# Optimization experiments

Measured on AMD Instinct MI355X. Metric: run time of the kernel, lower is better.

Reference implementation:

```python
import jax, jax.numpy as jnp
import numpy as np

BETA = 0.25
N_E = 4096
E_DIM = 64
B, T = 16, 1024


def setup_inputs() -> dict:
    key = jax.random.key(0)
    k1, k2 = jax.random.split(key)
    z = jax.random.normal(k1, (B, T, E_DIM), dtype=jnp.float32)
    # embedding.weight.data.uniform_(-1/n_e, 1/n_e)
    codebook = jax.random.uniform(k2, (N_E, E_DIM), dtype=jnp.float32,
                                  minval=-1.0 / N_E, maxval=1.0 / N_E)
    return {"z": z, "codebook": codebook}


def reference(z, codebook):
    # z: (B, T, e_dim), codebook: (n_e, e_dim)
    n_e, e_dim = codebook.shape
    zf = z.reshape(-1, e_dim)  # (N, e_dim)

    # d[n, k] = ||z_n||^2 + ||e_k||^2 - 2 z_n . e_k   -> (N, n_e)
    d = (jnp.sum(zf * zf, axis=1, keepdims=True)
         + jnp.sum(codebook * codebook, axis=1)
         - 2.0 * jnp.matmul(zf, codebook.T))

    idx = jnp.argmin(d, axis=1)                  # (N,) int
    z_q = codebook[idx].reshape(z.shape)         # (B, T, e_dim)

    sg = jax.lax.stop_gradient
    loss = jnp.mean((z_q - sg(z)) ** 2) + BETA * jnp.mean((sg(z_q) - z) ** 2)

    # straight-through estimator
    z_q_st = z + sg(z_q - z)

    # e_mean = mean over tokens of one-hot encodings == normalized code counts
    n_tokens = idx.shape[0]
    counts = jnp.zeros((n_e,), dtype=z.dtype).at[idx].add(1.0)
    e_mean = counts / n_tokens
    perplexity = jnp.exp(-jnp.sum(e_mean * jnp.log(e_mean + 1e-10)))

    return (loss, z_q_st, idx, perplexity)
```

## Files before the change

### kernel.cpp

```cpp
#include <hip/hip_runtime.h>
#include <math.h>

#define N_TOK   16384
#define EDIM    64
#define NE      4096
#define CHUNK   128
#define TPB     256
#define TOKPT   2
#define ZQ_OFF  1
#define IDX_OFF (1 + N_TOK * EDIM)
#define PERP_OFF (IDX_OFF + N_TOK)

typedef unsigned long long u64;
typedef float v2f __attribute__((ext_vector_type(2)));
typedef float v4f __attribute__((ext_vector_type(4)));

__global__ __launch_bounds__(256, 2) void dist_argmin_kernel(
    const float* __restrict__ z, const float* __restrict__ cb,
    u64* __restrict__ part, int* __restrict__ hist,
    float* __restrict__ lossAcc, int csl) {
    __shared__ float se[CHUNK * EDIM];
    __shared__ float sne[CHUNK];
    const int tid    = threadIdx.x;
    const int token0 = blockIdx.x * (TPB * TOKPT) + tid;
    const int token1 = token0 + TPB;
    const int slice  = blockIdx.y;

    if (slice == 0) {
        int gid = blockIdx.x * TPB + tid;
        if (gid < NE) hist[gid] = 0;
        if (gid == NE) lossAcc[0] = 0.0f;
    }

    v2f zp[EDIM];
    {
        const v4f* zp0 = (const v4f*)(z + (size_t)token0 * EDIM);
        const v4f* zp1 = (const v4f*)(z + (size_t)token1 * EDIM);
#pragma unroll
        for (int q = 0; q < 16; ++q) {
            v4f a = zp0[q], b = zp1[q];
            zp[4 * q + 0].x = a.x; zp[4 * q + 0].y = b.x;
            zp[4 * q + 1].x = a.y; zp[4 * q + 1].y = b.y;
            zp[4 * q + 2].x = a.z; zp[4 * q + 2].y = b.z;
            zp[4 * q + 3].x = a.w; zp[4 * q + 3].y = b.w;
        }
    }
    float tnz0, tnz1;
    {
#pragma clang fp contract(off)
        float r0[8], r1[8];
#pragma unroll
        for (int j = 0; j < 8; ++j) {
            float v0 = zp[j].x, v1 = zp[j].y;
            r0[j] = v0 * v0; r1[j] = v1 * v1;
        }
#pragma unroll
        for (int b = 8; b < 64; b += 8) {
#pragma unroll
            for (int j = 0; j < 8; ++j) {
                float v0 = zp[b + j].x, v1 = zp[b + j].y;
                r0[j] = r0[j] + v0 * v0; r1[j] = r1[j] + v1 * v1;
            }
        }
        tnz0 = ((r0[0] + r0[1]) + (r0[2] + r0[3])) + ((r0[4] + r0[5]) + (r0[6] + r0[7]));
        tnz1 = ((r1[0] + r1[1]) + (r1[2] + r1[3])) + ((r1[4] + r1[5]) + (r1[6] + r1[7]));
    }

    u64 best0 = ~0ull, best1 = ~0ull;
    const int kend = slice * csl + csl;
#pragma unroll 1
    for (int kbase = slice * csl; kbase < kend; kbase += CHUNK) {
        {
            const v4f* src = (const v4f*)(cb + (size_t)kbase * EDIM);
            v4f* dst = (v4f*)se;
#pragma unroll
            for (int r = 0; r < (CHUNK * EDIM / 4) / TPB; ++r)
                dst[r * TPB + tid] = src[r * TPB + tid];
        }
        if (tid < CHUNK) {
#pragma clang fp contract(off)
            const v4f* cr = (const v4f*)(cb + (size_t)(kbase + tid) * EDIM);
            float r[8];
            {
                v4f c0 = cr[0], c1 = cr[1];
                r[0] = c0.x * c0.x; r[1] = c0.y * c0.y;
                r[2] = c0.z * c0.z; r[3] = c0.w * c0.w;
                r[4] = c1.x * c1.x; r[5] = c1.y * c1.y;
                r[6] = c1.z * c1.z; r[7] = c1.w * c1.w;
            }
#pragma unroll
            for (int b = 1; b < 8; ++b) {
                v4f a = cr[2 * b], d = cr[2 * b + 1];
                r[0] = r[0] + a.x * a.x; r[1] = r[1] + a.y * a.y;
                r[2] = r[2] + a.z * a.z; r[3] = r[3] + a.w * a.w;
                r[4] = r[4] + d.x * d.x; r[5] = r[5] + d.y * d.y;
                r[6] = r[6] + d.z * d.z; r[7] = r[7] + d.w * d.w;
            }
            sne[tid] = ((r[0] + r[1]) + (r[2] + r[3])) + ((r[4] + r[5]) + (r[6] + r[7]));
        }
        __syncthreads();

#pragma unroll 1
        for (int k = 0; k < CHUNK; k += 2) {
            const v4f* e0 = (const v4f*)(se + (size_t)(k + 0) * EDIM);
            const v4f* e1 = (const v4f*)(se + (size_t)(k + 1) * EDIM);
            v2f a0 = {0.f, 0.f}, a1 = {0.f, 0.f};
#pragma unroll
            for (int q = 0; q < 16; ++q) {
                v4f A = e0[q], B = e1[q];
                v2f Alo = __builtin_shufflevector(A, A, 0, 1);
                v2f Ahi = __builtin_shufflevector(A, A, 2, 3);
                v2f Blo = __builtin_shufflevector(B, B, 0, 1);
                v2f Bhi = __builtin_shufflevector(B, B, 2, 3);
                asm("v_pk_fma_f32 %0, %1, %2, %0 op_sel:[0,0,0] op_sel_hi:[1,0,1]"
                    : "+v"(a0) : "v"(zp[4 * q + 0]), "v"(Alo));
                asm("v_pk_fma_f32 %0, %1, %2, %0 op_sel:[0,1,0] op_sel_hi:[1,1,1]"
                    : "+v"(a0) : "v"(zp[4 * q + 1]), "v"(Alo));
                asm("v_pk_fma_f32 %0, %1, %2, %0 op_sel:[0,0,0] op_sel_hi:[1,0,1]"
                    : "+v"(a0) : "v"(zp[4 * q + 2]), "v"(Ahi));
                asm("v_pk_fma_f32 %0, %1, %2, %0 op_sel:[0,1,0] op_sel_hi:[1,1,1]"
                    : "+v"(a0) : "v"(zp[4 * q + 3]), "v"(Ahi));
                asm("v_pk_fma_f32 %0, %1, %2, %0 op_sel:[0,0,0] op_sel_hi:[1,0,1]"
                    : "+v"(a1) : "v"(zp[4 * q + 0]), "v"(Blo));
                asm("v_pk_fma_f32 %0, %1, %2, %0 op_sel:[0,1,0] op_sel_hi:[1,1,1]"
                    : "+v"(a1) : "v"(zp[4 * q + 1]), "v"(Blo));
                asm("v_pk_fma_f32 %0, %1, %2, %0 op_sel:[0,0,0] op_sel_hi:[1,0,1]"
                    : "+v"(a1) : "v"(zp[4 * q + 2]), "v"(Bhi));
                asm("v_pk_fma_f32 %0, %1, %2, %0 op_sel:[0,1,0] op_sel_hi:[1,1,1]"
                    : "+v"(a1) : "v"(zp[4 * q + 3]), "v"(Bhi));
            }
            const float s0 = sne[k + 0], s1 = sne[k + 1];
            float t00 = __builtin_fmaf(-2.0f, a0.x, tnz0 + s0);
            float t01 = __builtin_fmaf(-2.0f, a1.x, tnz0 + s1);
            float t10 = __builtin_fmaf(-2.0f, a0.y, tnz1 + s0);
            float t11 = __builtin_fmaf(-2.0f, a1.y, tnz1 + s1);
            u64 p;
            p = ((u64)__float_as_uint(t00) << 32) | (u64)(kbase + k + 0); if (p < best0) best0 = p;
            p = ((u64)__float_as_uint(t01) << 32) | (u64)(kbase + k + 1); if (p < best0) best0 = p;
            p = ((u64)__float_as_uint(t10) << 32) | (u64)(kbase + k + 0); if (p < best1) best1 = p;
            p = ((u64)__float_as_uint(t11) << 32) | (u64)(kbase + k + 1); if (p < best1) best1 = p;
        }
        __syncthreads();
    }
    part[(size_t)slice * N_TOK + token0] = best0;
    part[(size_t)slice * N_TOK + token1] = best1;
}

__global__ __launch_bounds__(256) void reduce_gather_kernel(
    const float* __restrict__ z, const float* __restrict__ cb,
    const u64* __restrict__ part, int* __restrict__ hist,
    float* __restrict__ lossAcc, float* __restrict__ out, int nslice) {
    const int t = blockIdx.x * 256 + threadIdx.x;
    u64 best = part[t];
    for (int s = 1; s < nslice; ++s) {
        u64 p = part[(size_t)s * N_TOK + t];
        if (p < best) best = p;
    }
    const int idx = (int)(best & 0xFFFFFFFFull);
    out[IDX_OFF + t] = (float)idx;
    atomicAdd(&hist[idx], 1);

    const float4* ev = (const float4*)(cb + (size_t)idx * EDIM);
    const float4* zv = (const float4*)(z + (size_t)t * EDIM);
    float* o = out + ZQ_OFF + (size_t)t * EDIM;
    float acc = 0.0f;
#pragma unroll
    for (int j = 0; j < 16; ++j) {
        float4 e = ev[j], zz = zv[j];
        float d;
        d = e.x - zz.x; o[4 * j + 0] = zz.x + d; acc = __builtin_fmaf(d, d, acc);
        d = e.y - zz.y; o[4 * j + 1] = zz.y + d; acc = __builtin_fmaf(d, d, acc);
        d = e.z - zz.z; o[4 * j + 2] = zz.z + d; acc = __builtin_fmaf(d, d, acc);
        d = e.w - zz.w; o[4 * j + 3] = zz.w + d; acc = __builtin_fmaf(d, d, acc);
    }
    __shared__ float red[256];
    red[threadIdx.x] = acc;
    __syncthreads();
    for (int s = 128; s > 0; s >>= 1) {
        if (threadIdx.x < s) red[threadIdx.x] += red[threadIdx.x + s];
        __syncthreads();
    }
    if (threadIdx.x == 0) atomicAdd(lossAcc, red[0]);
}

__global__ __launch_bounds__(256) void finalize_kernel(
    const int* __restrict__ hist, const float* __restrict__ lossAcc,
    float* __restrict__ out) {
    __shared__ float red[256];
    float acc = 0.0f;
    for (int i = threadIdx.x; i < NE; i += 256) {
        float e = (float)hist[i] * (1.0f / 16384.0f);
        acc += e * logf(e + 1e-10f);
    }
    red[threadIdx.x] = acc;
    __syncthreads();
    for (int s = 128; s > 0; s >>= 1) {
        if (threadIdx.x < s) red[threadIdx.x] += red[threadIdx.x + s];
        __syncthreads();
    }
    if (threadIdx.x == 0) {
        out[PERP_OFF] = expf(-red[0]);
        float m = lossAcc[0] * (1.0f / 1048576.0f);
        out[0] = m + 0.25f * m;
    }
}

extern "C" void kernel_launch(void* const* d_in, const int* in_sizes, int n_in,
                              void* d_out, int out_size, void* d_ws, size_t ws_size,
                              hipStream_t stream) {
    const float* z  = (const float*)d_in[0];
    const float* cb = (const float*)d_in[1];
    float* out = (float*)d_out;

    const size_t need32 = (size_t)32 * N_TOK * 8 + (size_t)(NE + 1) * 4;
    const int nslice = (ws_size >= need32) ? 32 : 16;
    const int csl = NE / nslice;

    char* ws = (char*)d_ws;
    u64*   part    = (u64*)ws;
    int*   hist    = (int*)(ws + (size_t)nslice * N_TOK * 8);
    float* lossAcc = (float*)(hist + NE);

    hipLaunchKernelGGL(dist_argmin_kernel,
                       dim3(N_TOK / (TPB * TOKPT), nslice), dim3(TPB), 0, stream,
                       z, cb, part, hist, lossAcc, csl);
    hipLaunchKernelGGL(reduce_gather_kernel, dim3(64), dim3(256), 0, stream,
                       z, cb, part, hist, lossAcc, out, nslice);
    hipLaunchKernelGGL(finalize_kernel, dim3(1), dim3(256), 0, stream,
                       hist, lossAcc, out);
}
```

Before: 225.2 us.

## Register-block four tokens per thread and parallelize gather across quarter-rows

The distance kernel now holds four tokens per thread in registers instead of two. Each shared-memory codebook load therefore feeds twice as many packed FMAs. The chunk loop is dropped on the assumption that each slice covers exactly one CHUNK of codes. The reduce/gather kernel splits each token across four threads, each handling 16 elements, which gives more blocks and better-coalesced work. Risks: holding 256 z values per thread may exceed the VGPR budget under launch_bounds(256,2) and spill. The distance grid is halved, and the 16-slice fallback would skip half of each slice's codes.

```diff
diff --git a/kernel.cpp b/kernel.cpp
--- a/kernel.cpp
+++ b/kernel.cpp
@@ -6,7 +6,7 @@
 #define NE      4096
 #define CHUNK   128
 #define TPB     256
-#define TOKPT   2
+#define TOKPT   4
 #define ZQ_OFF  1
 #define IDX_OFF (1 + N_TOK * EDIM)
 #define PERP_OFF (IDX_OFF + N_TOK)
@@ -18,160 +18,190 @@
 __global__ __launch_bounds__(256, 2) void dist_argmin_kernel(
     const float* __restrict__ z, const float* __restrict__ cb,
     u64* __restrict__ part, int* __restrict__ hist,
-    float* __restrict__ lossAcc, int csl) {
+    float* __restrict__ lossAcc, int nslice) {
     __shared__ float se[CHUNK * EDIM];
     __shared__ float sne[CHUNK];
     const int tid    = threadIdx.x;
     const int token0 = blockIdx.x * (TPB * TOKPT) + tid;
-    const int token1 = token0 + TPB;
     const int slice  = blockIdx.y;
+    const int kb     = slice * (NE / nslice);
 
     if (slice == 0) {
         int gid = blockIdx.x * TPB + tid;
         if (gid < NE) hist[gid] = 0;
-        if (gid == NE) lossAcc[0] = 0.0f;
-    }
-
-    v2f zp[EDIM];
+        if (gid == 0) lossAcc[0] = 0.0f;
+    }
+
+    v2f zpA[EDIM], zpB[EDIM];
     {
-        const v4f* zp0 = (const v4f*)(z + (size_t)token0 * EDIM);
-        const v4f* zp1 = (const v4f*)(z + (size_t)token1 * EDIM);
+        const v4f* p0 = (const v4f*)(z + (size_t)(token0 + 0 * TPB) * EDIM);
+        const v4f* p1 = (const v4f*)(z + (size_t)(token0 + 1 * TPB) * EDIM);
+        const v4f* p2 = (const v4f*)(z + (size_t)(token0 + 2 * TPB) * EDIM);
+        const v4f* p3 = (const v4f*)(z + (size_t)(token0 + 3 * TPB) * EDIM);
 #pragma unroll
         for (int q = 0; q < 16; ++q) {
-            v4f a = zp0[q], b = zp1[q];
-            zp[4 * q + 0].x = a.x; zp[4 * q + 0].y = b.x;
-            zp[4 * q + 1].x = a.y; zp[4 * q + 1].y = b.y;
-            zp[4 * q + 2].x = a.z; zp[4 * q + 2].y = b.z;
-            zp[4 * q + 3].x = a.w; zp[4 * q + 3].y = b.w;
-        }
-    }
-    float tnz0, tnz1;
+            v4f a = p0[q], b = p1[q], c = p2[q], d = p3[q];
+            zpA[4 * q + 0].x = a.x; zpA[4 * q + 0].y = b.x;
+            zpA[4 * q + 1].x = a.y; zpA[4 * q + 1].y = b.y;
+            zpA[4 * q + 2].x = a.z; zpA[4 * q + 2].y = b.z;
+            zpA[4 * q + 3].x = a.w; zpA[4 * q + 3].y = b.w;
+            zpB[4 * q + 0].x = c.x; zpB[4 * q + 0].y = d.x;
+            zpB[4 * q + 1].x = c.y; zpB[4 * q + 1].y = d.y;
+            zpB[4 * q + 2].x = c.z; zpB[4 * q + 2].y = d.z;
+            zpB[4 * q + 3].x = c.w; zpB[4 * q + 3].y = d.w;
+        }
+    }
+    float tnz0, tnz1, tnz2, tnz3;
     {
 #pragma clang fp contract(off)
-        float r0[8], r1[8];
+        float r0[8], r1[8], r2[8], r3[8];
 #pragma unroll
         for (int j = 0; j < 8; ++j) {
-            float v0 = zp[j].x, v1 = zp[j].y;
-            r0[j] = v0 * v0; r1[j] = v1 * v1;
-        }
-#pragma unroll
-        for (int b = 8; b < 64; b += 8) {
+            float a = zpA[j].x, b = zpA[j].y, c = zpB[j].x, d = zpB[j].y;
+            r0[j] = a * a; r1[j] = b * b; r2[j] = c * c; r3[j] = d * d;
+        }
+#pragma unroll
+        for (int bb = 8; bb < 64; bb += 8) {
 #pragma unroll
             for (int j = 0; j < 8; ++j) {
-                float v0 = zp[b + j].x, v1 = zp[b + j].y;
-                r0[j] = r0[j] + v0 * v0; r1[j] = r1[j] + v1 * v1;
+                float a = zpA[bb + j].x, b = zpA[bb + j].y;
+                float c = zpB[bb + j].x, d = zpB[bb + j].y;
+                r0[j] = r0[j] + a * a; r1[j] = r1[j] + b * b;
+                r2[j] = r2[j] + c * c; r3[j] = r3[j] + d * d;
             }
         }
         tnz0 = ((r0[0] + r0[1]) + (r0[2] + r0[3])) + ((r0[4] + r0[5]) + (r0[6] + r0[7]));
         tnz1 = ((r1[0] + r1[1]) + (r1[2] + r1[3])) + ((r1[4] + r1[5]) + (r1[6] + r1[7]));
-    }
-
-    u64 best0 = ~0ull, best1 = ~0ull;
-    const int kend = slice * csl + csl;
+        tnz2 = ((r2[0] + r2[1]) + (r2[2] + r2[3])) + ((r2[4] + r2[5]) + (r2[6] + r2[7]));
+        tnz3 = ((r3[0] + r3[1]) + (r3[2] + r3[3])) + ((r3[4] + r3[5]) + (r3[6] + r3[7]));
+    }
+
+    {
+        const v4f* src = (const v4f*)(cb + (size_t)kb * EDIM);
+        v4f* dst = (v4f*)se;
+#pragma unroll
+        for (int r = 0; r < (CHUNK * EDIM / 4) / TPB; ++r)
+            dst[r * TPB + tid] = src[r * TPB + tid];
+    }
+    if (tid < CHUNK) {
+#pragma clang fp contract(off)
+        const v4f* cr = (const v4f*)(cb + (size_t)(kb + tid) * EDIM);
+        float r[8];
+        {
+            v4f c0 = cr[0], c1 = cr[1];
+            r[0] = c0.x * c0.x; r[1] = c0.y * c0.y;
+            r[2] = c0.z * c0.z; r[3] = c0.w * c0.w;
+            r[4] = c1.x * c1.x; r[5] = c1.y * c1.y;
+            r[6] = c1.z * c1.z; r[7] = c1.w * c1.w;
+        }
+#pragma unroll
+        for (int b = 1; b < 8; ++b) {
+            v4f a = cr[2 * b], d = cr[2 * b + 1];
+            r[0] = r[0] + a.x * a.x; r[1] = r[1] + a.y * a.y;
+            r[2] = r[2] + a.z * a.z; r[3] = r[3] + a.w * a.w;
+            r[4] = r[4] + d.x * d.x; r[5] = r[5] + d.y * d.y;
+            r[6] = r[6] + d.z * d.z; r[7] = r[7] + d.w * d.w;
+        }
+        sne[tid] = ((r[0] + r[1]) + (r[2] + r[3])) + ((r[4] + r[5]) + (r[6] + r[7]));
+    }
+    __syncthreads();
+
+    u64 best0 = ~0ull, best1 = ~0ull, best2 = ~0ull, best3 = ~0ull;
 #pragma unroll 1
-    for (int kbase = slice * csl; kbase < kend; kbase += CHUNK) {
-        {
-            const v4f* src = (const v4f*)(cb + (size_t)kbase * EDIM);
-            v4f* dst = (v4f*)se;
-#pragma unroll
-            for (int r = 0; r < (CHUNK * EDIM / 4) / TPB; ++r)
-                dst[r * TPB + tid] = src[r * TPB + tid];
-        }
-        if (tid < CHUNK) {
-#pragma clang fp contract(off)
-            const v4f* cr = (const v4f*)(cb + (size_t)(kbase + tid) * EDIM);
-            float r[8];
-            {
-                v4f c0 = cr[0], c1 = cr[1];
-                r[0] = c0.x * c0.x; r[1] = c0.y * c0.y;
-                r[2] = c0.z * c0.z; r[3] = c0.w * c0.w;
-                r[4] = c1.x * c1.x; r[5] = c1.y * c1.y;
-                r[6] = c1.z * c1.z; r[7] = c1.w * c1.w;
-            }
-#pragma unroll
-            for (int b = 1; b < 8; ++b) {
-                v4f a = cr[2 * b], d = cr[2 * b + 1];
-                r[0] = r[0] + a.x * a.x; r[1] = r[1] + a.y * a.y;
-                r[2] = r[2] + a.z * a.z; r[3] = r[3] + a.w * a.w;
-                r[4] = r[4] + d.x * d.x; r[5] = r[5] + d.y * d.y;
-                r[6] = r[6] + d.z * d.z; r[7] = r[7] + d.w * d.w;
-            }
-            sne[tid] = ((r[0] + r[1]) + (r[2] + r[3])) + ((r[4] + r[5]) + (r[6] + r[7]));
-        }
-        __syncthreads();
-
-#pragma unroll 1
-        for (int k = 0; k < CHUNK; k += 2) {
-            const v4f* e0 = (const v4f*)(se + (size_t)(k + 0) * EDIM);
-            const v4f* e1 = (const v4f*)(se + (size_t)(k + 1) * EDIM);
-            v2f a0 = {0.f, 0.f}, a1 = {0.f, 0.f};
-#pragma unroll
-            for (int q = 0; q < 16; ++q) {
-                v4f A = e0[q], B = e1[q];
-                v2f Alo = __builtin_shufflevector(A, A, 0, 1);
-                v2f Ahi = __builtin_shufflevector(A, A, 2, 3);
-                v2f Blo = __builtin_shufflevector(B, B, 0, 1);
-                v2f Bhi = __builtin_shufflevector(B, B, 2, 3);
-                asm("v_pk_fma_f32 %0, %1, %2, %0 op_sel:[0,0,0] op_sel_hi:[1,0,1]"
-                    : "+v"(a0) : "v"(zp[4 * q + 0]), "v"(Alo));
-                asm("v_pk_fma_f32 %0, %1, %2, %0 op_sel:[0,1,0] op_sel_hi:[1,1,1]"
-                    : "+v"(a0) : "v"(zp[4 * q + 1]), "v"(Alo));
-                asm("v_pk_fma_f32 %0, %1, %2, %0 op_sel:[0,0,0] op_sel_hi:[1,0,1]"
-                    : "+v"(a0) : "v"(zp[4 * q + 2]), "v"(Ahi));
-                asm("v_pk_fma_f32 %0, %1, %2, %0 op_sel:[0,1,0] op_sel_hi:[1,1,1]"
-                    : "+v"(a0) : "v"(zp[4 * q + 3]), "v"(Ahi));
-                asm("v_pk_fma_f32 %0, %1, %2, %0 op_sel:[0,0,0] op_sel_hi:[1,0,1]"
-                    : "+v"(a1) : "v"(zp[4 * q + 0]), "v"(Blo));
-                asm("v_pk_fma_f32 %0, %1, %2, %0 op_sel:[0,1,0] op_sel_hi:[1,1,1]"
-                    : "+v"(a1) : "v"(zp[4 * q + 1]), "v"(Blo));
-                asm("v_pk_fma_f32 %0, %1, %2, %0 op_sel:[0,0,0] op_sel_hi:[1,0,1]"
-                    : "+v"(a1) : "v"(zp[4 * q + 2]), "v"(Bhi));
-                asm("v_pk_fma_f32 %0, %1, %2, %0 op_sel:[0,1,0] op_sel_hi:[1,1,1]"
-                    : "+v"(a1) : "v"(zp[4 * q + 3]), "v"(Bhi));
-            }
-            const float s0 = sne[k + 0], s1 = sne[k + 1];
-            float t00 = __builtin_fmaf(-2.0f, a0.x, tnz0 + s0);
-            float t01 = __builtin_fmaf(-2.0f, a1.x, tnz0 + s1);
-            float t10 = __builtin_fmaf(-2.0f, a0.y, tnz1 + s0);
-            float t11 = __builtin_fmaf(-2.0f, a1.y, tnz1 + s1);
-            u64 p;
-            p = ((u64)__float_as_uint(t00) << 32) | (u64)(kbase + k + 0); if (p < best0) best0 = p;
-            p = ((u64)__float_as_uint(t01) << 32) | (u64)(kbase + k + 1); if (p < best0) best0 = p;
-            p = ((u64)__float_as_uint(t10) << 32) | (u64)(kbase + k + 0); if (p < best1) best1 = p;
-            p = ((u64)__float_as_uint(t11) << 32) | (u64)(kbase + k + 1); if (p < best1) best1 = p;
-        }
-        __syncthreads();
-    }
-    part[(size_t)slice * N_TOK + token0] = best0;
-    part[(size_t)slice * N_TOK + token1] = best1;
+    for (int k = 0; k < CHUNK; k += 2) {
+        const v4f* e0 = (const v4f*)(se + (size_t)(k + 0) * EDIM);
+        const v4f* e1 = (const v4f*)(se + (size_t)(k + 1) * EDIM);
+        v2f aA0 = {0.f, 0.f}, aA1 = {0.f, 0.f};
+        v2f aB0 = {0.f, 0.f}, aB1 = {0.f, 0.f};
+#pragma unroll
+        for (int q = 0; q < 16; ++q) {
+            v4f A = e0[q], B = e1[q];
+            v2f Alo = __builtin_shufflevector(A, A, 0, 1);
+            v2f Ahi = __builtin_shufflevector(A, A, 2, 3);
+            v2f Blo = __builtin_shufflevector(B, B, 0, 1);
+            v2f Bhi = __builtin_shufflevector(B, B, 2, 3);
+            asm("v_pk_fma_f32 %0, %1, %2, %0 op_sel:[0,0,0] op_sel_hi:[1,0,1]"
+                : "+v"(aA0) : "v"(zpA[4 * q + 0]), "v"(Alo));
+            asm("v_pk_fma_f32 %0, %1, %2, %0 op_sel:[0,1,0] op_sel_hi:[1,1,1]"
+                : "+v"(aA0) : "v"(zpA[4 * q + 1]), "v"(Alo));
+            asm("v_pk_fma_f32 %0, %1, %2, %0 op_sel:[0,0,0] op_sel_hi:[1,0,1]"
+                : "+v"(aA0) : "v"(zpA[4 * q + 2]), "v"(Ahi));
+            asm("v_pk_fma_f32 %0, %1, %2, %0 op_sel:[0,1,0] op_sel_hi:[1,1,1]"
+                : "+v"(aA0) : "v"(zpA[4 * q + 3]), "v"(Ahi));
+            asm("v_pk_fma_f32 %0, %1, %2, %0 op_sel:[0,0,0] op_sel_hi:[1,0,1]"
+                : "+v"(aA1) : "v"(zpA[4 * q + 0]), "v"(Blo));
+            asm("v_pk_fma_f32 %0, %1, %2, %0 op_sel:[0,1,0] op_sel_hi:[1,1,1]"
+                : "+v"(aA1) : "v"(zpA[4 * q + 1]), "v"(Blo));
+            asm("v_pk_fma_f32 %0, %1, %2, %0 op_sel:[0,0,0] op_sel_hi:[1,0,1]"
+                : "+v"(aA1) : "v"(zpA[4 * q + 2]), "v"(Bhi));
+            asm("v_pk_fma_f32 %0, %1, %2, %0 op_sel:[0,1,0] op_sel_hi:[1,1,1]"
+                : "+v"(aA1) : "v"(zpA[4 * q + 3]), "v"(Bhi));
+            asm("v_pk_fma_f32 %0, %1, %2, %0 op_sel:[0,0,0] op_sel_hi:[1,0,1]"
+                : "+v"(aB0) : "v"(zpB[4 * q + 0]), "v"(Alo));
+            asm("v_pk_fma_f32 %0, %1, %2, %0 op_sel:[0,1,0] op_sel_hi:[1,1,1]"
+                : "+v"(aB0) : "v"(zpB[4 * q + 1]), "v"(Alo));
+            asm("v_pk_fma_f32 %0, %1, %2, %0 op_sel:[0,0,0] op_sel_hi:[1,0,1]"
+                : "+v"(aB0) : "v"(zpB[4 * q + 2]), "v"(Ahi));
+            asm("v_pk_fma_f32 %0, %1, %2, %0 op_sel:[0,1,0] op_sel_hi:[1,1,1]"
+                : "+v"(aB0) : "v"(zpB[4 * q + 3]), "v"(Ahi));
+            asm("v_pk_fma_f32 %0, %1, %2, %0 op_sel:[0,0,0] op_sel_hi:[1,0,1]"
+                : "+v"(aB1) : "v"(zpB[4 * q + 0]), "v"(Blo));
+            asm("v_pk_fma_f32 %0, %1, %2, %0 op_sel:[0,1,0] op_sel_hi:[1,1,1]"
+                : "+v"(aB1) : "v"(zpB[4 * q + 1]), "v"(Blo));
+            asm("v_pk_fma_f32 %0, %1, %2, %0 op_sel:[0,0,0] op_sel_hi:[1,0,1]"
+                : "+v"(aB1) : "v"(zpB[4 * q + 2]), "v"(Bhi));
+            asm("v_pk_fma_f32 %0, %1, %2, %0 op_sel:[0,1,0] op_sel_hi:[1,1,1]"
+                : "+v"(aB1) : "v"(zpB[4 * q + 3]), "v"(Bhi));
+        }
+        const float s0 = sne[k + 0], s1 = sne[k + 1];
+        float t00 = __builtin_fmaf(-2.f, aA0.x, tnz0 + s0);
+        float t10 = __builtin_fmaf(-2.f, aA0.y, tnz1 + s0);
+        float t20 = __builtin_fmaf(-2.f, aB0.x, tnz2 + s0);
+        float t30 = __builtin_fmaf(-2.f, aB0.y, tnz3 + s0);
+        float t01 = __builtin_fmaf(-2.f, aA1.x, tnz0 + s1);
+        float t11 = __builtin_fmaf(-2.f, aA1.y, tnz1 + s1);
+        float t21 = __builtin_fmaf(-2.f, aB1.x, tnz2 + s1);
+        float t31 = __builtin_fmaf(-2.f, aB1.y, tnz3 + s1);
+        u64 p;
+        p = ((u64)__float_as_uint(t00) << 32) | (u64)(kb + k + 0); if (p < best0) best0 = p;
+        p = ((u64)__float_as_uint(t01) << 32) | (u64)(kb + k + 1); if (p < best0) best0 = p;
+        p = ((u64)__float_as_uint(t10) << 32) | (u64)(kb + k + 0); if (p < best1) best1 = p;
+        p = ((u64)__float_as_uint(t11) << 32) | (u64)(kb + k + 1); if (p < best1) best1 = p;
+        p = ((u64)__float_as_uint(t20) << 32) | (u64)(kb + k + 0); if (p < best2) best2 = p;
+        p = ((u64)__float_as_uint(t21) << 32) | (u64)(kb + k + 1); if (p < best2) best2 = p;
+        p = ((u64)__float_as_uint(t30) << 32) | (u64)(kb + k + 0); if (p < best3) best3 = p;
+        p = ((u64)__float_as_uint(t31) << 32) | (u64)(kb + k + 1); if (p < best3) best3 = p;
+    }
+    part[(size_t)slice * N_TOK + token0 + 0 * TPB] = best0;
+    part[(size_t)slice * N_TOK + token0 + 1 * TPB] = best1;
+    part[(size_t)slice * N_TOK + token0 + 2 * TPB] = best2;
+    part[(size_t)slice * N_TOK + token0 + 3 * TPB] = best3;
 }
 
 __global__ __launch_bounds__(256) void reduce_gather_kernel(
     const float* __restrict__ z, const float* __restrict__ cb,
     const u64* __restrict__ part, int* __restrict__ hist,
     float* __restrict__ lossAcc, float* __restrict__ out, int nslice) {
-    const int t = blockIdx.x * 256 + threadIdx.x;
-    u64 best = part[t];
+    const int id = blockIdx.x * 256 + threadIdx.x;
+    const int tok = id >> 2, q = id & 3;
+    u64 best = part[tok];
     for (int s = 1; s < nslice; ++s) {
-        u64 p = part[(size_t)s * N_TOK + t];
+        u64 p = part[(size_t)s * N_TOK + tok];
         if (p < best) best = p;
     }
     const int idx = (int)(best & 0xFFFFFFFFull);
-    out[IDX_OFF + t] = (float)idx;
-    atomicAdd(&hist[idx], 1);
-
-    const float4* ev = (const float4*)(cb + (size_t)idx * EDIM);
-    const float4* zv = (const float4*)(z + (size_t)t * EDIM);
-    float* o = out + ZQ_OFF + (size_t)t * EDIM;
-    float acc = 0.0f;
-#pragma unroll
-    for (int j = 0; j < 16; ++j) {
-        float4 e = ev[j], zz = zv[j];
-        float d;
-        d = e.x - zz.x; o[4 * j + 0] = zz.x + d; acc = __builtin_fmaf(d, d, acc);
-        d = e.y - zz.y; o[4 * j + 1] = zz.y + d; acc = __builtin_fmaf(d, d, acc);
-        d = e.z - zz.z; o[4 * j + 2] = zz.z + d; acc = __builtin_fmaf(d, d, acc);
-        d = e.w - zz.w; o[4 * j + 3] = zz.w + d; acc = __builtin_fmaf(d, d, acc);
+    if (q == 0) { out[IDX_OFF + tok] = (float)idx; atomicAdd(&hist[idx], 1); }
+
+    const float* ev = cb + (size_t)idx * EDIM + 16 * q;
+    const float* zv = z + (size_t)tok * EDIM + 16 * q;
+    float* o = out + ZQ_OFF + (size_t)tok * EDIM + 16 * q;
+    float acc = 0.f;
+#pragma unroll
+    for (int i = 0; i < 16; ++i) {
+        float e = ev[i], zz = zv[i];
+        float d = e - zz;
+        o[i] = zz + d;
+        acc = __builtin_fmaf(d, d, acc);
     }
     __shared__ float red[256];
     red[threadIdx.x] = acc;
@@ -214,7 +244,6 @@
 
     const size_t need32 = (size_t)32 * N_TOK * 8 + (size_t)(NE + 1) * 4;
     const int nslice = (ws_size >= need32) ? 32 : 16;
-    const int csl = NE / nslice;
 
     char* ws = (char*)d_ws;
     u64*   part    = (u64*)ws;
@@ -223,8 +252,8 @@
 
     hipLaunchKernelGGL(dist_argmin_kernel,
                        dim3(N_TOK / (TPB * TOKPT), nslice), dim3(TPB), 0, stream,
-                       z, cb, part, hist, lossAcc, csl);
-    hipLaunchKernelGGL(reduce_gather_kernel, dim3(64), dim3(256), 0, stream,
+                       z, cb, part, hist, lossAcc, nslice);
+    hipLaunchKernelGGL(reduce_gather_kernel, dim3(256), dim3(256), 0, stream,
                        z, cb, part, hist, lossAcc, out, nslice);
     hipLaunchKernelGGL(finalize_kernel, dim3(1), dim3(256), 0, stream,
                        hist, lossAcc, out);
```

New measurement: 359.4 us. 59.5% more time.

## Read codebook via scalar loads, precompute code norms, widen gather parallelism

Applied to the files above, without the earlier changes.

The distance kernel no longer stages codebook chunks in LDS behind barriers. Codebook rows are block-uniform, so it reads them through scalar (SGPR) loads that feed packed FMAs directly. Code norms are now computed once by a new prep kernel, which also zeroes the histogram and loss accumulator. The slice count drops from 32 to 16, and the gather kernel uses four threads per token for more parallelism. This removes LDS traffic and synchronisation, but the hot loop now depends on scalar-cache latency, and there are fewer blocks plus one extra launch.

```diff
diff --git a/kernel.cpp b/kernel.cpp
--- a/kernel.cpp
+++ b/kernel.cpp
@@ -4,7 +4,6 @@
 #define N_TOK   16384
 #define EDIM    64
 #define NE      4096
-#define CHUNK   128
 #define TPB     256
 #define TOKPT   2
 #define ZQ_OFF  1
@@ -15,30 +14,40 @@
 typedef float v2f __attribute__((ext_vector_type(2)));
 typedef float v4f __attribute__((ext_vector_type(4)));
 
+__global__ __launch_bounds__(256) void prep_kernel(
+    const float* __restrict__ cb, float* __restrict__ ne,
+    int* __restrict__ hist, float* __restrict__ lossAcc) {
+#pragma clang fp contract(off)
+    const int i = blockIdx.x * 256 + threadIdx.x;
+    hist[i] = 0;
+    if (i == 0) lossAcc[0] = 0.0f;
+    const float* row = cb + (size_t)i * EDIM;
+    float r[8];
+#pragma unroll
+    for (int j = 0; j < 8; ++j) { float v = row[j]; r[j] = v * v; }
+#pragma unroll
+    for (int b = 8; b < 64; b += 8) {
+#pragma unroll
+        for (int j = 0; j < 8; ++j) { float v = row[b + j]; r[j] = r[j] + v * v; }
+    }
+    ne[i] = ((r[0] + r[1]) + (r[2] + r[3])) + ((r[4] + r[5]) + (r[6] + r[7]));
+}
+
 __global__ __launch_bounds__(256, 2) void dist_argmin_kernel(
     const float* __restrict__ z, const float* __restrict__ cb,
-    u64* __restrict__ part, int* __restrict__ hist,
-    float* __restrict__ lossAcc, int csl) {
-    __shared__ float se[CHUNK * EDIM];
-    __shared__ float sne[CHUNK];
+    const float* __restrict__ ne, u64* __restrict__ part, int csl) {
     const int tid    = threadIdx.x;
     const int token0 = blockIdx.x * (TPB * TOKPT) + tid;
     const int token1 = token0 + TPB;
-    const int slice  = blockIdx.y;
-
-    if (slice == 0) {
-        int gid = blockIdx.x * TPB + tid;
-        if (gid < NE) hist[gid] = 0;
-        if (gid == NE) lossAcc[0] = 0.0f;
-    }
+    const int kb     = __builtin_amdgcn_readfirstlane(blockIdx.y * csl);
 
     v2f zp[EDIM];
     {
-        const v4f* zp0 = (const v4f*)(z + (size_t)token0 * EDIM);
-        const v4f* zp1 = (const v4f*)(z + (size_t)token1 * EDIM);
+        const v4f* p0 = (const v4f*)(z + (size_t)token0 * EDIM);
+        const v4f* p1 = (const v4f*)(z + (size_t)token1 * EDIM);
 #pragma unroll
         for (int q = 0; q < 16; ++q) {
-            v4f a = zp0[q], b = zp1[q];
+            v4f a = p0[q], b = p1[q];
             zp[4 * q + 0].x = a.x; zp[4 * q + 0].y = b.x;
             zp[4 * q + 1].x = a.y; zp[4 * q + 1].y = b.y;
             zp[4 * q + 2].x = a.z; zp[4 * q + 2].y = b.z;
@@ -51,15 +60,15 @@
         float r0[8], r1[8];
 #pragma unroll
         for (int j = 0; j < 8; ++j) {
-            float v0 = zp[j].x, v1 = zp[j].y;
-            r0[j] = v0 * v0; r1[j] = v1 * v1;
+            float a = zp[j].x, b = zp[j].y;
+            r0[j] = a * a; r1[j] = b * b;
         }
 #pragma unroll
-        for (int b = 8; b < 64; b += 8) {
+        for (int bb = 8; bb < 64; bb += 8) {
 #pragma unroll
             for (int j = 0; j < 8; ++j) {
-                float v0 = zp[b + j].x, v1 = zp[b + j].y;
-                r0[j] = r0[j] + v0 * v0; r1[j] = r1[j] + v1 * v1;
+                float a = zp[bb + j].x, b = zp[bb + j].y;
+                r0[j] = r0[j] + a * a; r1[j] = r1[j] + b * b;
             }
         }
         tnz0 = ((r0[0] + r0[1]) + (r0[2] + r0[3])) + ((r0[4] + r0[5]) + (r0[6] + r0[7]));
@@ -67,111 +76,64 @@
     }
 
     u64 best0 = ~0ull, best1 = ~0ull;
-    const int kend = slice * csl + csl;
 #pragma unroll 1
-    for (int kbase = slice * csl; kbase < kend; kbase += CHUNK) {
-        {
-            const v4f* src = (const v4f*)(cb + (size_t)kbase * EDIM);
-            v4f* dst = (v4f*)se;
+    for (int kk = 0; kk < csl; kk += 2) {
+        const int k = kb + kk;
+        const u64* e0 = (const u64*)(cb + (size_t)(k + 0) * EDIM);
+        const u64* e1 = (const u64*)(cb + (size_t)(k + 1) * EDIM);
+        v2f a0 = {0.f, 0.f}, a1 = {0.f, 0.f};
 #pragma unroll
-            for (int r = 0; r < (CHUNK * EDIM / 4) / TPB; ++r)
-                dst[r * TPB + tid] = src[r * TPB + tid];
+        for (int jp = 0; jp < 32; ++jp) {
+            u64 w0 = e0[jp];
+            u64 w1 = e1[jp];
+            asm("v_pk_fma_f32 %0, %1, %2, %0 op_sel:[0,0,0] op_sel_hi:[1,0,1]"
+                : "+v"(a0) : "v"(zp[2 * jp + 0]), "s"(w0));
+            asm("v_pk_fma_f32 %0, %1, %2, %0 op_sel:[0,1,0] op_sel_hi:[1,1,1]"
+                : "+v"(a0) : "v"(zp[2 * jp + 1]), "s"(w0));
+            asm("v_pk_fma_f32 %0, %1, %2, %0 op_sel:[0,0,0] op_sel_hi:[1,0,1]"
+                : "+v"(a1) : "v"(zp[2 * jp + 0]), "s"(w1));
+            asm("v_pk_fma_f32 %0, %1, %2, %0 op_sel:[0,1,0] op_sel_hi:[1,1,1]"
+                : "+v"(a1) : "v"(zp[2 * jp + 1]), "s"(w1));
         }
-        if (tid < CHUNK) {
-#pragma clang fp contract(off)
-            const v4f* cr = (const v4f*)(cb + (size_t)(kbase + tid) * EDIM);
-            float r[8];
-            {
-                v4f c0 = cr[0], c1 = cr[1];
-                r[0] = c0.x * c0.x; r[1] = c0.y * c0.y;
-                r[2] = c0.z * c0.z; r[3] = c0.w * c0.w;
-                r[4] = c1.x * c1.x; r[5] = c1.y * c1.y;
-                r[6] = c1.z * c1.z; r[7] = c1.w * c1.w;
-            }
-#pragma unroll
-            for (int b = 1; b < 8; ++b) {
-                v4f a = cr[2 * b], d = cr[2 * b + 1];
-                r[0] = r[0] + a.x * a.x; r[1] = r[1] + a.y * a.y;
-                r[2] = r[2] + a.z * a.z; r[3] = r[3] + a.w * a.w;
-                r[4] = r[4] + d.x * d.x; r[5] = r[5] + d.y * d.y;
-                r[6] = r[6] + d.z * d.z; r[7] = r[7] + d.w * d.w;
-            }
-            sne[tid] = ((r[0] + r[1]) + (r[2] + r[3])) + ((r[4] + r[5]) + (r[6] + r[7]));
-        }
-        __syncthreads();
-
-#pragma unroll 1
-        for (int k = 0; k < CHUNK; k += 2) {
-            const v4f* e0 = (const v4f*)(se + (size_t)(k + 0) * EDIM);
-            const v4f* e1 = (const v4f*)(se + (size_t)(k + 1) * EDIM);
-            v2f a0 = {0.f, 0.f}, a1 = {0.f, 0.f};
-#pragma unroll
-            for (int q = 0; q < 16; ++q) {
-                v4f A = e0[q], B = e1[q];
-                v2f Alo = __builtin_shufflevector(A, A, 0, 1);
-                v2f Ahi = __builtin_shufflevector(A, A, 2, 3);
-                v2f Blo = __builtin_shufflevector(B, B, 0, 1);
-                v2f Bhi = __builtin_shufflevector(B, B, 2, 3);
-                asm("v_pk_fma_f32 %0, %1, %2, %0 op_sel:[0,0,0] op_sel_hi:[1,0,1]"
-                    : "+v"(a0) : "v"(zp[4 * q + 0]), "v"(Alo));
-                asm("v_pk_fma_f32 %0, %1, %2, %0 op_sel:[0,1,0] op_sel_hi:[1,1,1]"
-                    : "+v"(a0) : "v"(zp[4 * q + 1]), "v"(Alo));
-                asm("v_pk_fma_f32 %0, %1, %2, %0 op_sel:[0,0,0] op_sel_hi:[1,0,1]"
-                    : "+v"(a0) : "v"(zp[4 * q + 2]), "v"(Ahi));
-                asm("v_pk_fma_f32 %0, %1, %2, %0 op_sel:[0,1,0] op_sel_hi:[1,1,1]"
-                    : "+v"(a0) : "v"(zp[4 * q + 3]), "v"(Ahi));
-                asm("v_pk_fma_f32 %0, %1, %2, %0 op_sel:[0,0,0] op_sel_hi:[1,0,1]"
-                    : "+v"(a1) : "v"(zp[4 * q + 0]), "v"(Blo));
-                asm("v_pk_fma_f32 %0, %1, %2, %0 op_sel:[0,1,0] op_sel_hi:[1,1,1]"
-                    : "+v"(a1) : "v"(zp[4 * q + 1]), "v"(Blo));
-                asm("v_pk_fma_f32 %0, %1, %2, %0 op_sel:[0,0,0] op_sel_hi:[1,0,1]"
-                    : "+v"(a1) : "v"(zp[4 * q + 2]), "v"(Bhi));
-                asm("v_pk_fma_f32 %0, %1, %2, %0 op_sel:[0,1,0] op_sel_hi:[1,1,1]"
-                    : "+v"(a1) : "v"(zp[4 * q + 3]), "v"(Bhi));
-            }
-            const float s0 = sne[k + 0], s1 = sne[k + 1];
-            float t00 = __builtin_fmaf(-2.0f, a0.x, tnz0 + s0);
-            float t01 = __builtin_fmaf(-2.0f, a1.x, tnz0 + s1);
-            float t10 = __builtin_fmaf(-2.0f, a0.y, tnz1 + s0);
-            float t11 = __builtin_fmaf(-2.0f, a1.y, tnz1 + s1);
-            u64 p;
-            p = ((u64)__float_as_uint(t00) << 32) | (u64)(kbase + k + 0); if (p < best0) best0 = p;
-            p = ((u64)__float_as_uint(t01) << 32) | (u64)(kbase + k + 1); if (p < best0) best0 = p;
-            p = ((u64)__float_as_uint(t10) << 32) | (u64)(kbase + k + 0); if (p < best1) best1 = p;
-            p = ((u64)__float_as_uint(t11) << 32) | (u64)(kbase + k + 1); if (p < best1) best1 = p;
-        }
-        __syncthreads();
+        const float s0 = ne[k], s1 = ne[k + 1];
+        float t00 = __builtin_fmaf(-2.f, a0.x, tnz0 + s0);
+        float t10 = __builtin_fmaf(-2.f, a0.y, tnz1 + s0);
+        float t01 = __builtin_fmaf(-2.f, a1.x, tnz0 + s1);
+        float t11 = __builtin_fmaf(-2.f, a1.y, tnz1 + s1);
+        u64 p;
+        p = ((u64)__float_as_uint(t00) << 32) | (u64)(k + 0); if (p < best0) best0 = p;
+        p = ((u64)__float_as_uint(t01) << 32) | (u64)(k + 1); if (p < best0) best0 = p;
+        p = ((u64)__float_as_uint(t10) << 32) | (u64)(k + 0); if (p < best1) best1 = p;
+        p = ((u64)__float_as_uint(t11) << 32) | (u64)(k + 1); if (p < best1) best1 = p;
     }
-    part[(size_t)slice * N_TOK + token0] = best0;
-    part[(size_t)slice * N_TOK + token1] = best1;
+    part[(size_t)blockIdx.y * N_TOK + token0] = best0;
+    part[(size_t)blockIdx.y * N_TOK + token1] = best1;
 }
 
 __global__ __launch_bounds__(256) void reduce_gather_kernel(
     const float* __restrict__ z, const float* __restrict__ cb,
     const u64* __restrict__ part, int* __restrict__ hist,
     float* __restrict__ lossAcc, float* __restrict__ out, int nslice) {
-    const int t = blockIdx.x * 256 + threadIdx.x;
-    u64 best = part[t];
+    const int id = blockIdx.x * 256 + threadIdx.x;
+    const int tok = id >> 2, q = id & 3;
+    u64 best = part[tok];
     for (int s = 1; s < nslice; ++s) {
-        u64 p = part[(size_t)s * N_TOK + t];
+        u64 p = part[(size_t)s * N_TOK + tok];
         if (p < best) best = p;
     }
     const int idx = (int)(best & 0xFFFFFFFFull);
-    out[IDX_OFF + t] = (float)idx;
-    atomicAdd(&hist[idx], 1);
+    if (q == 0) { out[IDX_OFF + tok] = (float)idx; atomicAdd(&hist[idx], 1); }
 
-    const float4* ev = (const float4*)(cb + (size_t)idx * EDIM);
-    const float4* zv = (const float4*)(z + (size_t)t * EDIM);
-    float* o = out + ZQ_OFF + (size_t)t * EDIM;
-    float acc = 0.0f;
+    const float* ev = cb + (size_t)idx * EDIM + 16 * q;
+    const float* zv = z + (size_t)tok * EDIM + 16 * q;
+    float* o = out + ZQ_OFF + (size_t)tok * EDIM + 16 * q;
+    float acc = 0.f;
 #pragma unroll
-    for (int j = 0; j < 16; ++j) {
-        float4 e = ev[j], zz = zv[j];
-        float d;
-        d = e.x - zz.x; o[4 * j + 0] = zz.x + d; acc = __builtin_fmaf(d, d, acc);
-        d = e.y - zz.y; o[4 * j + 1] = zz.y + d; acc = __builtin_fmaf(d, d, acc);
-        d = e.z - zz.z; o[4 * j + 2] = zz.z + d; acc = __builtin_fmaf(d, d, acc);
-        d = e.w - zz.w; o[4 * j + 3] = zz.w + d; acc = __builtin_fmaf(d, d, acc);
+    for (int i = 0; i < 16; ++i) {
+        float e = ev[i], zz = zv[i];
+        float d = e - zz;
+        o[i] = zz + d;
+        acc = __builtin_fmaf(d, d, acc);
     }
     __shared__ float red[256];
     red[threadIdx.x] = acc;
@@ -212,19 +174,22 @@
     const float* cb = (const float*)d_in[1];
     float* out = (float*)d_out;
 
-    const size_t need32 = (size_t)32 * N_TOK * 8 + (size_t)(NE + 1) * 4;
-    const int nslice = (ws_size >= need32) ? 32 : 16;
+    const size_t need16 = (size_t)16 * N_TOK * 8 + (size_t)NE * 8 + 64;
+    const int nslice = (ws_size >= need16) ? 16 : 8;
     const int csl = NE / nslice;
 
     char* ws = (char*)d_ws;
     u64*   part    = (u64*)ws;
-    int*   hist    = (int*)(ws + (size_t)nslice * N_TOK * 8);
+    float* ne      = (float*)(ws + (size_t)nslice * N_TOK * 8);
+    int*   hist    = (int*)(ne + NE);
     float* lossAcc = (float*)(hist + NE);
 
+    hipLaunchKernelGGL(prep_kernel, dim3(16), dim3(256), 0, stream,
+                       cb, ne, hist, lossAcc);
     hipLaunchKernelGGL(dist_argmin_kernel,
                        dim3(N_TOK / (TPB * TOKPT), nslice), dim3(TPB), 0, stream,
-                       z, cb, part, hist, lossAcc, csl);
-    hipLaunchKernelGGL(reduce_gather_kernel, dim3(64), dim3(256), 0, stream,
+                       z, cb, ne, part, csl);
+    hipLaunchKernelGGL(reduce_gather_kernel, dim3(256), dim3(256), 0, stream,
                        z, cb, part, hist, lossAcc, out, nslice);
     hipLaunchKernelGGL(finalize_kernel, dim3(1), dim3(256), 0, stream,
                        hist, lossAcc, out);
```

Result: slower. 264.1 us (+17.3%).
